# Kernel optimization log

Hardware: AMD Instinct MI355X
Metric: run time of the kernel (lower is better)

Reference implementation:

```python
import jax, jax.numpy as jnp
import numpy as np

N = 50000      # nodes
E = 1600000    # edges
D = 128        # input_dim
H = 128        # hidden_dim
C = 10         # n_class
G = 512        # number of graphs (max(idx)+1)
LRELU_ALPHA = 0.05
BN_EPS = 1e-5


def setup_inputs() -> dict:
    key = jax.random.key(0)
    ks = jax.random.split(key, 10)
    x_in = jax.random.normal(ks[0], (N, D), dtype=jnp.float32)
    edge_index = jax.random.randint(ks[1], (2, E), 0, N, dtype=jnp.int32)
    idx = jnp.sort(jax.random.randint(ks[2], (N,), 0, G, dtype=jnp.int32))

    def lin(k, shape, fan_in):
        return jax.random.normal(k, shape, dtype=jnp.float32) / np.sqrt(fan_in).astype(np.float32)

    fc_w = lin(ks[3], (H, D), D)        # GATLayer.fc weight
    a1 = lin(ks[4], (H,), 2 * H)        # a weight, src half
    a2 = lin(ks[5], (H,), 2 * H)        # a weight, dst half
    fc1_w = lin(ks[6], (H, H), H)
    fc1_b = jnp.zeros((H,), jnp.float32)
    fc2_w = lin(ks[7], (C, H), H)
    fc2_b = jnp.zeros((C,), jnp.float32)
    gamma = jnp.ones((H,), jnp.float32)  # BatchNorm weight
    beta = jnp.zeros((H,), jnp.float32)  # BatchNorm bias
    return {"x_in": x_in, "edge_index": edge_index, "idx": idx,
            "fc_w": fc_w, "a1": a1, "a2": a2,
            "fc1_w": fc1_w, "fc1_b": fc1_b, "fc2_w": fc2_w, "fc2_b": fc2_b,
            "gamma": gamma, "beta": beta}


def reference(x_in, edge_index, idx, fc_w, a1, a2, fc1_w, fc1_b, fc2_w, fc2_b, gamma, beta):
    # input standardization (torch.std is unbiased -> ddof=1)
    x = (x_in - jnp.mean(x_in)) / jnp.std(x_in, ddof=1)

    # ---- GAT layer ----
    z = x @ fc_w.T                              # [N, H]
    src, dst = edge_index[0], edge_index[1]
    # a([z_src ; z_dst]) == z_src@a1 + z_dst@a2  (avoids materializing [E, 2H])
    s1 = z @ a1                                  # [N]
    s2 = z @ a2                                  # [N]
    e = s1[src] + s2[dst]                        # [E]
    e = jnp.where(e >= 0, e, LRELU_ALPHA * e)    # LeakyReLU(0.05)
    h = jnp.exp(e)
    h_sum = jax.ops.segment_sum(h, src, num_segments=N)   # edge-softmax denom per src row
    alpha = h / h_sum[src]                       # [E]
    # sparse.mm(adj_att, z): out[src] += alpha * z[dst]
    out = jax.ops.segment_sum(alpha[:, None] * z[dst], src, num_segments=N)  # [N, H]

    x = jax.nn.relu(out)
    # dropout: identity (eval / deterministic reference)

    # sum pooling per graph
    pooled = jax.ops.segment_sum(x, idx, num_segments=G)   # [G, H]

    # BatchNorm1d (training-mode batch statistics, biased var)
    mu = jnp.mean(pooled, axis=0)
    var = jnp.var(pooled, axis=0)
    xb = (pooled - mu) / jnp.sqrt(var + BN_EPS) * gamma + beta

    x = jax.nn.relu(xb @ fc1_w.T + fc1_b)
    logits = x @ fc2_w.T + fc2_b
    return jax.nn.log_softmax(logits, axis=1)
```

## Files before the change

### kernel.cpp

```cpp
#include <hip/hip_runtime.h>

#define NN 50000
#define NE 1600000
#define DD 128
#define HH 128
#define CC 10
#define GG 512
#define LRELU_A 0.05f
#define BN_EPS 1e-5f

#define TT 256
#define EPT (NE / TT)
#define NB 196
#define NPB 256
#define KNODE 8
#define STB 1024

typedef unsigned int u32;
typedef unsigned short u16;
typedef unsigned char u8;
typedef __attribute__((ext_vector_type(8))) short bf16x8;
typedef __attribute__((ext_vector_type(4))) float f32x4;

__device__ __forceinline__ u16 f2bf(float f) {
    u32 u = __float_as_uint(f);
    u32 r = u + 0x7FFFu + ((u >> 16) & 1u);
    return (u16)(r >> 16);
}
__device__ __forceinline__ float bf2f(u32 lo16) {
    return __uint_as_float(lo16 << 16);
}

__global__ __launch_bounds__(256) void k_front(const int* __restrict__ src,
                                               const float* __restrict__ x,
                                               u16* __restrict__ cnt_b,
                                               u8* __restrict__ rank_e,
                                               float* __restrict__ pooled,
                                               double* __restrict__ pst) {
    __shared__ u32 h[NB];
    __shared__ double ls[4], lss[4];
    int bid = blockIdx.x, tid = threadIdx.x;
    if (bid < TT) {
        for (int i = tid; i < NB; i += 256) h[i] = 0;
        pooled[bid * 256 + tid] = 0.f;
        __syncthreads();
        int e0 = bid * EPT;
        for (int i = tid; i < EPT; i += 256) {
            int b = src[e0 + i] >> 8;
            u32 old = atomicAdd(&h[b], 1u);
            rank_e[e0 + i] = (u8)old;
        }
        __syncthreads();
        for (int i = tid; i < NB; i += 256) cnt_b[bid * NB + i] = (u16)h[i];
    } else {
        int sb = bid - TT;
        const int M4 = NN * DD / 4;
        double s = 0.0, ss = 0.0;
        for (int i = sb * 256 + tid; i < M4; i += STB * 256) {
            float4 v = reinterpret_cast<const float4*>(x)[i];
            s  += (double)v.x + (double)v.y + (double)v.z + (double)v.w;
            ss += (double)v.x * v.x + (double)v.y * v.y + (double)v.z * v.z +
                  (double)v.w * v.w;
        }
        for (int d = 32; d; d >>= 1) { s += __shfl_down(s, d); ss += __shfl_down(ss, d); }
        int lane = tid & 63, w = tid >> 6;
        if (lane == 0) { ls[w] = s; lss[w] = ss; }
        __syncthreads();
        if (tid == 0) {
            pst[2 * sb]     = ls[0] + ls[1] + ls[2] + ls[3];
            pst[2 * sb + 1] = lss[0] + lss[1] + lss[2] + lss[3];
        }
    }
}

__global__ __launch_bounds__(256) void k_mid(const u16* __restrict__ cnt_b,
                                             const double* __restrict__ pst,
                                             const float* __restrict__ fc_w,
                                             u16* __restrict__ rel_b,
                                             int* __restrict__ base_b,
                                             float* __restrict__ wsum,
                                             float* __restrict__ musig,
                                             u16* __restrict__ wbf) {
    int t = threadIdx.x;
    if (blockIdx.x == 0) {
        __shared__ int sm[256];
        int b = t;
        int run = 0;
        if (b < NB) {
            for (int tt = 0; tt < TT; ++tt) {
                int c = cnt_b[tt * NB + b];
                rel_b[tt * NB + b] = (u16)run;
                run += c;
            }
        }
        sm[b] = (b < NB) ? run : 0;
        __syncthreads();
        int v = sm[b];
        for (int d = 1; d < 256; d <<= 1) {
            int x = 0;
            if (b >= d) x = sm[b - d];
            __syncthreads();
            if (b >= d) sm[b] += x;
            __syncthreads();
        }
        if (b < NB) base_b[b] = sm[b] - v;
        if (b == NB - 1) base_b[NB] = sm[b];
    } else {
        __shared__ double rs[256], rss[256];
        double s  = pst[2 * t] + pst[2 * (t + 256)] + pst[2 * (t + 512)] + pst[2 * (t + 768)];
        double ss = pst[2 * t + 1] + pst[2 * (t + 256) + 1] +
                    pst[2 * (t + 512) + 1] + pst[2 * (t + 768) + 1];
        rs[t] = s; rss[t] = ss;
        __syncthreads();
        for (int d = 128; d; d >>= 1) {
            if (t < d) { rs[t] += rs[t + d]; rss[t] += rss[t + d]; }
            __syncthreads();
        }
        if (t == 0) {
            double M = (double)NN * DD;
            double mean = rs[0] / M;
            double var  = (rss[0] - rs[0] * rs[0] / M) / (M - 1.0);
            musig[0] = (float)mean;
            musig[1] = (float)(1.0 / sqrt(var));
        }
        for (int i = t; i < DD * HH; i += 256) wbf[i] = f2bf(fc_w[i]);
        if (t < 128) {
            float acc = 0.f;
            for (int k = 0; k < DD; ++k)
                acc += bf2f(f2bf(fc_w[t * DD + k]));
            wsum[t] = acc;
        }
    }
}

#define XP 136
__global__ __launch_bounds__(256) void k_big(const int* __restrict__ src,
                                             const int* __restrict__ dst,
                                             const u16* __restrict__ rel_b,
                                             const u8* __restrict__ rank_e,
                                             const int* __restrict__ base_b,
                                             u32* __restrict__ ebuf,
                                             const float* __restrict__ x,
                                             const u16* __restrict__ wbf,
                                             const float* __restrict__ wsum,
                                             const float* __restrict__ musig,
                                             const float* __restrict__ a1,
                                             const float* __restrict__ a2,
                                             u32* __restrict__ zbf,
                                             float* __restrict__ s1,
                                             float* __restrict__ s2) {
    __shared__ u16 xls[64 * XP];
    int bid = blockIdx.x, tid = threadIdx.x;

    if (bid < TT) {
        int e0 = bid * EPT;
        for (int i = tid; i < EPT; i += 256) {
            int s = src[e0 + i];
            int b = s >> 8;
            int pos = base_b[b] + (int)rel_b[bid * NB + b] + (int)rank_e[e0 + i];
            ebuf[pos] = ((u32)dst[e0 + i] << 8) | (u32)(s & 255);
        }
        return;
    }

    int row0 = (bid - TT) * 64;
    for (int i = tid; i < 64 * 32; i += 256) {
        int r = i >> 5, m = i & 31;
        int gr = row0 + r;
        float4 v = (gr < NN) ? reinterpret_cast<const float4*>(x)[gr * 32 + m]
                             : make_float4(0.f, 0.f, 0.f, 0.f);
        u32 p0 = ((u32)f2bf(v.y) << 16) | f2bf(v.x);
        u32 p1 = ((u32)f2bf(v.w) << 16) | f2bf(v.z);
        *reinterpret_cast<uint2*>(&xls[r * XP + m * 4]) = make_uint2(p0, p1);
    }
    __syncthreads();

    int w = tid >> 6, l = tid & 63;
    int lrow = l & 15, lk = l >> 4;

    bf16x8 af[4];
    #pragma unroll
    for (int kc = 0; kc < 4; ++kc)
        af[kc] = *reinterpret_cast<const bf16x8*>(
            &xls[(w * 16 + lrow) * XP + kc * 32 + lk * 8]);

    f32x4 acc[8];
    #pragma unroll
    for (int nt = 0; nt < 8; ++nt) acc[nt] = (f32x4){0.f, 0.f, 0.f, 0.f};

    #pragma unroll
    for (int nt = 0; nt < 8; ++nt) {
        #pragma unroll
        for (int kc = 0; kc < 4; ++kc) {
            bf16x8 bfr = *reinterpret_cast<const bf16x8*>(
                &wbf[(nt * 16 + lrow) * DD + kc * 32 + lk * 8]);
            acc[nt] = __builtin_amdgcn_mfma_f32_16x16x32_bf16(af[kc], bfr,
                                                              acc[nt], 0, 0, 0);
        }
    }
    __syncthreads();

    float mu = musig[0], isig = musig[1];
    #pragma unroll
    for (int nt = 0; nt < 8; ++nt) {
        int col = nt * 16 + lrow;
        float wsc = wsum[col];
        #pragma unroll
        for (int r = 0; r < 4; ++r) {
            int lr = w * 16 + lk * 4 + r;
            float z = (acc[nt][r] - mu * wsc) * isig;
            xls[lr * XP + col] = f2bf(z);
        }
    }
    __syncthreads();

    {
        int r = tid >> 2, q = tid & 3;
        int gr = row0 + r;
        const uint4* lz = reinterpret_cast<const uint4*>(&xls[r * XP + q * 32]);
        uint4 c0 = lz[0], c1 = lz[1], c2 = lz[2], c3 = lz[3];
        if (gr < NN) {
            uint4* zb = reinterpret_cast<uint4*>(zbf) + gr * 16 + q * 4;
            zb[0] = c0; zb[1] = c1; zb[2] = c2; zb[3] = c3;
        }
        u32 wd[16] = {c0.x, c0.y, c0.z, c0.w, c1.x, c1.y, c1.z, c1.w,
                      c2.x, c2.y, c2.z, c2.w, c3.x, c3.y, c3.z, c3.w};
        const float4* A14 = reinterpret_cast<const float4*>(a1 + q * 32);
        const float4* A24 = reinterpret_cast<const float4*>(a2 + q * 32);
        float p1 = 0.f, p2 = 0.f;
        #pragma unroll
        for (int j = 0; j < 8; ++j) {
            float4 va1 = A14[j], va2 = A24[j];
            u32 wlo = wd[2 * j], whi = wd[2 * j + 1];
            float z0 = bf2f(wlo & 0xFFFFu), z1 = bf2f(wlo >> 16);
            float z2 = bf2f(whi & 0xFFFFu), z3 = bf2f(whi >> 16);
            p1 += z0 * va1.x + z1 * va1.y + z2 * va1.z + z3 * va1.w;
            p2 += z0 * va2.x + z1 * va2.y + z2 * va2.z + z3 * va2.w;
        }
        p1 += __shfl_down(p1, 2, 4); p1 += __shfl_down(p1, 1, 4);
        p2 += __shfl_down(p2, 2, 4); p2 += __shfl_down(p2, 1, 4);
        if (q == 0 && gr < NN) { s1[gr] = p1; s2[gr] = p2; }
    }
}

__global__ __launch_bounds__(256) void k_bcsr(const u32* __restrict__ ebuf,
                                              const int* __restrict__ base_b,
                                              const float* __restrict__ s1,
                                              const float* __restrict__ s2,
                                              int* __restrict__ off,
                                              u32* __restrict__ dst_s) {
    __shared__ u32 hist[NPB];
    __shared__ u32 cur[NPB];
    __shared__ int sm[256];
    int b = blockIdx.x, tid = threadIdx.x;
    int ebase = base_b[b], eend = base_b[b + 1];
    int m = eend - ebase;
    hist[tid] = 0;
    __syncthreads();
    for (int i = tid; i < m; i += 256)
        atomicAdd(&hist[ebuf[ebase + i] & 255u], 1u);
    __syncthreads();
    int v = (int)hist[tid];
    sm[tid] = v;
    __syncthreads();
    for (int d = 1; d < 256; d <<= 1) {
        int x = 0;
        if (tid >= d) x = sm[tid - d];
        __syncthreads();
        if (tid >= d) sm[tid] += x;
        __syncthreads();
    }
    int st = sm[tid] - v;
    cur[tid] = (u32)st;
    int n = b * NPB + tid;
    if (n < NN) off[n] = ebase + st;
    if (b == NB - 1 && tid == 0) off[NN] = NE;
    __syncthreads();
    for (int i = tid; i < m; i += 256) {
        u32 e = ebuf[ebase + i];
        int ls = (int)(e & 255u);
        int dn = (int)(e >> 8);
        int p = (int)atomicAdd(&cur[ls], 1u);
        float ev = s1[b * NPB + ls] + s2[dn];
        ev = (ev >= 0.f) ? ev : LRELU_A * ev;
        float h = __expf(ev);
        dst_s[ebase + p] = ((u32)dn << 16) | (u32)f2bf(h);
    }
}

__global__ __launch_bounds__(256) void k_aggregate(const u32* __restrict__ zbf,
                                                   const int* __restrict__ off,
                                                   const u32* __restrict__ dst_s,
                                                   const int* __restrict__ idx,
                                                   float* __restrict__ pooled) {
    int wave = (blockIdx.x * 256 + threadIdx.x) >> 6;
    int lane = threadIdx.x & 63;
    int n0 = wave * KNODE;
    if (n0 >= NN) return;
    int n1 = n0 + KNODE;
    if (n1 > NN) n1 = NN;

    float pool0 = 0.f, pool1 = 0.f;
    int curg = idx[n0];

    for (int node = n0; node < n1; ++node) {
        int g = idx[node];
        if (g != curg) {
            atomicAdd(&pooled[curg * HH + lane * 2], pool0);
            atomicAdd(&pooled[curg * HH + lane * 2 + 1], pool1);
            pool0 = 0.f; pool1 = 0.f;
            curg = g;
        }
        int j0 = off[node], j1 = off[node + 1];
        float acc0 = 0.f, acc1 = 0.f, hsl = 0.f;

        for (int b = j0; b < j1; b += 64) {
            int cnt = j1 - b;
            if (cnt > 64) cnt = 64;
            int jj = b + ((lane < cnt) ? lane : 0);
            int ul = (int)dst_s[jj];
            if (lane < cnt) hsl += __uint_as_float((u32)ul << 16);
            int k = 0;
            for (; k + 8 <= cnt; k += 8) {
                int eu[8]; u32 uu[8];
                #pragma unroll
                for (int q = 0; q < 8; ++q) eu[q] = __shfl(ul, k + q);
                #pragma unroll
                for (int q = 0; q < 8; ++q)
                    uu[q] = zbf[(((u32)eu[q] >> 16) << 6) | lane];
                #pragma unroll
                for (int q = 0; q < 8; ++q) {
                    float hq = __uint_as_float((u32)eu[q] << 16);
                    acc0 += hq * __uint_as_float(uu[q] << 16);
                    acc1 += hq * __uint_as_float(uu[q] & 0xFFFF0000u);
                }
            }
            for (; k + 4 <= cnt; k += 4) {
                int eu[4]; u32 uu[4];
                #pragma unroll
                for (int q = 0; q < 4; ++q) eu[q] = __shfl(ul, k + q);
                #pragma unroll
                for (int q = 0; q < 4; ++q)
                    uu[q] = zbf[(((u32)eu[q] >> 16) << 6) | lane];
                #pragma unroll
                for (int q = 0; q < 4; ++q) {
                    float hq = __uint_as_float((u32)eu[q] << 16);
                    acc0 += hq * __uint_as_float(uu[q] << 16);
                    acc1 += hq * __uint_as_float(uu[q] & 0xFFFF0000u);
                }
            }
            for (; k < cnt; ++k) {
                int e = __shfl(ul, k);
                float hk = __uint_as_float((u32)e << 16);
                u32 u = zbf[(((u32)e >> 16) << 6) | lane];
                acc0 += hk * __uint_as_float(u << 16);
                acc1 += hk * __uint_as_float(u & 0xFFFF0000u);
            }
        }
        float hs = hsl;
        #pragma unroll
        for (int d = 32; d; d >>= 1) hs += __shfl_xor(hs, d);
        float inv = (hs > 0.f) ? 1.f / hs : 0.f;
        pool0 += fmaxf(acc0 * inv, 0.f);
        pool1 += fmaxf(acc1 * inv, 0.f);
    }
    atomicAdd(&pooled[curg * HH + lane * 2], pool0);
    atomicAdd(&pooled[curg * HH + lane * 2 + 1], pool1);
}

__global__ __launch_bounds__(128) void k_head(const float* __restrict__ pooled,
                                              const float* __restrict__ gamma,
                                              const float* __restrict__ beta,
                                              const float* __restrict__ fc1w,
                                              const float* __restrict__ fc1b,
                                              const float* __restrict__ fc2w,
                                              const float* __restrict__ fc2b,
                                              float* __restrict__ out) {
    __shared__ __align__(16) float xb[128];
    __shared__ __align__(16) float h1[128];
    __shared__ float lg[16];
    int g = blockIdx.x;
    int t = threadIdx.x;
    float s = 0.f, ss = 0.f;
    #pragma unroll 8
    for (int q = 0; q < GG; ++q) {
        float v = pooled[q * HH + t];
        s += v;
        ss += v * v;
    }
    float mean = s / GG;
    float var  = ss / GG - mean * mean;
    float sc = gamma[t] * rsqrtf(var + BN_EPS);
    xb[t] = pooled[g * HH + t] * sc + (beta[t] - mean * sc);
    __syncthreads();
    float acc = 0.f;
    const float4* wr = reinterpret_cast<const float4*>(&fc1w[t * HH]);
    #pragma unroll 8
    for (int k = 0; k < 32; ++k) {
        float4 w4 = wr[k];
        float4 xv = *reinterpret_cast<const float4*>(&xb[k * 4]);
        acc += w4.x * xv.x + w4.y * xv.y + w4.z * xv.z + w4.w * xv.w;
    }
    acc += fc1b[t];
    h1[t] = (acc > 0.f) ? acc : 0.f;
    __syncthreads();
    if (t < CC) {
        float a = 0.f;
        const float4* w2 = reinterpret_cast<const float4*>(&fc2w[t * HH]);
        #pragma unroll 8
        for (int k = 0; k < 32; ++k) {
            float4 w4 = w2[k];
            float4 hv = *reinterpret_cast<const float4*>(&h1[k * 4]);
            a += w4.x * hv.x + w4.y * hv.y + w4.z * hv.z + w4.w * hv.w;
        }
        lg[t] = a + fc2b[t];
    }
    __syncthreads();
    if (t == 0) {
        float mx = lg[0];
        for (int c = 1; c < CC; ++c) mx = fmaxf(mx, lg[c]);
        float se = 0.f;
        for (int c = 0; c < CC; ++c) se += __expf(lg[c] - mx);
        float lse = mx + logf(se);
        for (int c = 0; c < CC; ++c) out[g * CC + c] = lg[c] - lse;
    }
}

extern "C" void kernel_launch(void* const* d_in, const int* in_sizes, int n_in,
                              void* d_out, int out_size, void* d_ws, size_t ws_size,
                              hipStream_t stream) {
    const float* x_in  = (const float*)d_in[0];
    const int*   eidx  = (const int*)d_in[1];
    const int*   src   = eidx;
    const int*   dst   = eidx + NE;
    const int*   idx   = (const int*)d_in[2];
    const float* fc_w  = (const float*)d_in[3];
    const float* a1    = (const float*)d_in[4];
    const float* a2    = (const float*)d_in[5];
    const float* fc1w  = (const float*)d_in[6];
    const float* fc1b  = (const float*)d_in[7];
    const float* fc2w  = (const float*)d_in[8];
    const float* fc2b  = (const float*)d_in[9];
    const float* gamma = (const float*)d_in[10];
    const float* beta  = (const float*)d_in[11];
    float* out = (float*)d_out;

    char* p = (char*)d_ws;
    auto alloc = [&](size_t bytes) {
        char* r = p;
        p += (bytes + 255) & ~(size_t)255;
        return r;
    };
    double* pst    = (double*)alloc((size_t)STB * 2 * sizeof(double));
    float*  wsum   = (float*)alloc(HH * sizeof(float));
    float*  musig  = (float*)alloc(4 * sizeof(float));
    u16*    wbf    = (u16*)alloc((size_t)DD * HH * sizeof(u16));
    u16*    cnt_b  = (u16*)alloc((size_t)TT * NB * sizeof(u16));
    u16*    rel_b  = (u16*)alloc((size_t)TT * NB * sizeof(u16));
    u8*     rank_e = (u8*)alloc((size_t)NE * sizeof(u8));
    int*    base_b = (int*)alloc((NB + 1) * sizeof(int));
    u32*    ebuf   = (u32*)alloc((size_t)NE * sizeof(u32));
    int*    off    = (int*)alloc((NN + 1) * sizeof(int));
    u32*    dst_s  = (u32*)alloc((size_t)NE * sizeof(u32));
    u32*    zbf    = (u32*)alloc((size_t)NN * (HH / 2) * sizeof(u32));
    float*  s1     = (float*)alloc(NN * sizeof(float));
    float*  s2     = (float*)alloc(NN * sizeof(float));
    float*  pooled = (float*)alloc((size_t)GG * HH * sizeof(float));

    k_front<<<TT + STB, 256, 0, stream>>>(src, x_in, cnt_b, rank_e, pooled, pst);
    k_mid<<<2, 256, 0, stream>>>(cnt_b, pst, fc_w, rel_b, base_b, wsum, musig, wbf);
    int gemm_blocks = (NN + 63) / 64;
    k_big<<<TT + gemm_blocks, 256, 0, stream>>>(src, dst, rel_b, rank_e, base_b,
                                                ebuf, x_in, wbf, wsum, musig,
                                                a1, a2, zbf, s1, s2);
    k_bcsr<<<NB, 256, 0, stream>>>(ebuf, base_b, s1, s2, off, dst_s);
    int nwaves = (NN + KNODE - 1) / KNODE;
    int nblocks = (nwaves + 3) / 4;
    k_aggregate<<<nblocks, 256, 0, stream>>>(zbf, off, dst_s, idx, pooled);
    k_head<<<GG, 128, 0, stream>>>(pooled, gamma, beta, fc1w, fc1b, fc2w, fc2b, out);
}
```

Measured before the change: 171.4 us.

## Replace global per-edge rank buffer with LDS-local bucket sort before edge scatter

k_front no longer writes a per-edge rank byte array; it only builds per-block bucket histograms. The scatter blocks in k_big rebuild the histogram in shared memory, prefix-scan it, and bucket-sort the block's edges into LDS. They then write them to the global edge buffer in bucket order, so stores land in contiguous runs. This removes the global write and read of the rank array and turns scattered global writes into mostly grouped ones. The cost is a second read of src, extra shared atomics and scan barriers, and a larger static shared allocation that also applies to the GEMM blocks and may lower their occupancy.

Result: no change. 174.0 us (+1.5%).

```diff
diff --git a/kernel.cpp b/kernel.cpp
--- a/kernel.cpp
+++ b/kernel.cpp
@@ -34,7 +34,6 @@
 __global__ __launch_bounds__(256) void k_front(const int* __restrict__ src,
                                                const float* __restrict__ x,
                                                u16* __restrict__ cnt_b,
-                                               u8* __restrict__ rank_e,
                                                float* __restrict__ pooled,
                                                double* __restrict__ pst) {
     __shared__ u32 h[NB];
@@ -45,11 +44,8 @@
         pooled[bid * 256 + tid] = 0.f;
         __syncthreads();
         int e0 = bid * EPT;
-        for (int i = tid; i < EPT; i += 256) {
-            int b = src[e0 + i] >> 8;
-            u32 old = atomicAdd(&h[b], 1u);
-            rank_e[e0 + i] = (u8)old;
-        }
+        for (int i = tid; i < EPT; i += 256)
+            atomicAdd(&h[src[e0 + i] >> 8], 1u);
         __syncthreads();
         for (int i = tid; i < NB; i += 256) cnt_b[bid * NB + i] = (u16)h[i];
     } else {
@@ -134,10 +130,10 @@
 }
 
 #define XP 136
+#define SHWORDS (EPT + NB + NB + 256)
 __global__ __launch_bounds__(256) void k_big(const int* __restrict__ src,
                                              const int* __restrict__ dst,
                                              const u16* __restrict__ rel_b,
-                                             const u8* __restrict__ rank_e,
                                              const int* __restrict__ base_b,
                                              u32* __restrict__ ebuf,
                                              const float* __restrict__ x,
@@ -149,20 +145,50 @@
                                              u32* __restrict__ zbf,
                                              float* __restrict__ s1,
                                              float* __restrict__ s2) {
-    __shared__ u16 xls[64 * XP];
+    __shared__ __align__(16) u32 shmem[SHWORDS];
     int bid = blockIdx.x, tid = threadIdx.x;
 
     if (bid < TT) {
+        u32* eloc = shmem;
+        u32* hcur = shmem + EPT;
+        int* tpl  = (int*)(shmem + EPT + NB);
+        int* sm2  = (int*)(shmem + EPT + NB + NB);
         int e0 = bid * EPT;
+        for (int i = tid; i < NB; i += 256) hcur[i] = 0;
+        __syncthreads();
+        for (int i = tid; i < EPT; i += 256)
+            atomicAdd(&hcur[src[e0 + i] >> 8], 1u);
+        __syncthreads();
+        int b = tid;
+        int v = (b < NB) ? (int)hcur[b] : 0;
+        sm2[tid] = v;
+        __syncthreads();
+        for (int d = 1; d < 256; d <<= 1) {
+            int xv = 0;
+            if (tid >= d) xv = sm2[tid - d];
+            __syncthreads();
+            if (tid >= d) sm2[tid] += xv;
+            __syncthreads();
+        }
+        if (b < NB) { tpl[b] = sm2[tid] - v; hcur[b] = (u32)(sm2[tid] - v); }
+        __syncthreads();
         for (int i = tid; i < EPT; i += 256) {
             int s = src[e0 + i];
-            int b = s >> 8;
-            int pos = base_b[b] + (int)rel_b[bid * NB + b] + (int)rank_e[e0 + i];
-            ebuf[pos] = ((u32)dst[e0 + i] << 8) | (u32)(s & 255);
+            u32 pos = atomicAdd(&hcur[s >> 8], 1u);
+            eloc[pos] = ((u32)dst[e0 + i] << 16) | (u32)s;
+        }
+        __syncthreads();
+        for (int i = tid; i < EPT; i += 256) {
+            u32 e = eloc[i];
+            int s = (int)(e & 0xFFFFu);
+            int b2 = s >> 8;
+            int gpos = base_b[b2] + (int)rel_b[bid * NB + b2] + (i - tpl[b2]);
+            ebuf[gpos] = ((e >> 16) << 8) | (u32)(s & 255);
         }
         return;
     }
 
+    u16* xls = (u16*)shmem;
     int row0 = (bid - TT) * 64;
     for (int i = tid; i < 64 * 32; i += 256) {
         int r = i >> 5, m = i & 31;
@@ -457,7 +483,6 @@
     u16*    wbf    = (u16*)alloc((size_t)DD * HH * sizeof(u16));
     u16*    cnt_b  = (u16*)alloc((size_t)TT * NB * sizeof(u16));
     u16*    rel_b  = (u16*)alloc((size_t)TT * NB * sizeof(u16));
-    u8*     rank_e = (u8*)alloc((size_t)NE * sizeof(u8));
     int*    base_b = (int*)alloc((NB + 1) * sizeof(int));
     u32*    ebuf   = (u32*)alloc((size_t)NE * sizeof(u32));
     int*    off    = (int*)alloc((NN + 1) * sizeof(int));
@@ -467,10 +492,10 @@
     float*  s2     = (float*)alloc(NN * sizeof(float));
     float*  pooled = (float*)alloc((size_t)GG * HH * sizeof(float));
 
-    k_front<<<TT + STB, 256, 0, stream>>>(src, x_in, cnt_b, rank_e, pooled, pst);
+    k_front<<<TT + STB, 256, 0, stream>>>(src, x_in, cnt_b, pooled, pst);
     k_mid<<<2, 256, 0, stream>>>(cnt_b, pst, fc_w, rel_b, base_b, wsum, musig, wbf);
     int gemm_blocks = (NN + 63) / 64;
-    k_big<<<TT + gemm_blocks, 256, 0, stream>>>(src, dst, rel_b, rank_e, base_b,
+    k_big<<<TT + gemm_blocks, 256, 0, stream>>>(src, dst, rel_b, base_b,
                                                 ebuf, x_in, wbf, wsum, musig,
                                                 a1, a2, zbf, s1, s2);
     k_bcsr<<<NB, 256, 0, stream>>>(ebuf, base_b, s1, s2, off, dst_s);
```

## Fuse block CSR build and neighbor aggregation into one LDS-resident kernel

Applied to the files above, without the earlier changes.

Replaces the separate CSR-building kernel and aggregation kernel with one 1024-thread kernel per 256-node block. Each block buckets its edges and computes the attention weights into shared memory, then aggregates straight from that local sorted edge list. This removes the global write and re-read of the sorted edge array, the offset array and one launch. In exchange the aggregation runs on only 196 large blocks, which is fewer than the number of compute units and means fewer waves to hide gather latency. It also assumes each block has at most 8832 edges, with no bounds check.

Result: no change. 171.5 us (+0.0%).

```diff
diff --git a/kernel.cpp b/kernel.cpp
--- a/kernel.cpp
+++ b/kernel.cpp
@@ -13,7 +13,7 @@
 #define EPT (NE / TT)
 #define NB 196
 #define NPB 256
-#define KNODE 8
+#define EMAXB 8832
 #define STB 1024
 
 typedef unsigned int u32;
@@ -243,67 +243,67 @@
     }
 }
 
-__global__ __launch_bounds__(256) void k_bcsr(const u32* __restrict__ ebuf,
-                                              const int* __restrict__ base_b,
-                                              const float* __restrict__ s1,
-                                              const float* __restrict__ s2,
-                                              int* __restrict__ off,
-                                              u32* __restrict__ dst_s) {
+__global__ __launch_bounds__(1024) void k_agg2(const u32* __restrict__ ebuf,
+                                               const int* __restrict__ base_b,
+                                               const float* __restrict__ s1,
+                                               const float* __restrict__ s2,
+                                               const u32* __restrict__ zbf,
+                                               const int* __restrict__ idx,
+                                               float* __restrict__ pooled) {
+    __shared__ u32 eloc[EMAXB];
     __shared__ u32 hist[NPB];
     __shared__ u32 cur[NPB];
-    __shared__ int sm[256];
+    __shared__ int sm[NPB];
+    __shared__ int off_l[NPB + 1];
     int b = blockIdx.x, tid = threadIdx.x;
-    int ebase = base_b[b], eend = base_b[b + 1];
-    int m = eend - ebase;
-    hist[tid] = 0;
-    __syncthreads();
-    for (int i = tid; i < m; i += 256)
+    int ebase = base_b[b];
+    int m = base_b[b + 1] - ebase;
+
+    if (tid < NPB) hist[tid] = 0;
+    __syncthreads();
+    for (int i = tid; i < m; i += 1024)
         atomicAdd(&hist[ebuf[ebase + i] & 255u], 1u);
     __syncthreads();
-    int v = (int)hist[tid];
-    sm[tid] = v;
-    __syncthreads();
-    for (int d = 1; d < 256; d <<= 1) {
+    if (tid < NPB) sm[tid] = (int)hist[tid];
+    __syncthreads();
+    for (int d = 1; d < NPB; d <<= 1) {
         int x = 0;
-        if (tid >= d) x = sm[tid - d];
-        __syncthreads();
-        if (tid >= d) sm[tid] += x;
-        __syncthreads();
-    }
-    int st = sm[tid] - v;
-    cur[tid] = (u32)st;
-    int n = b * NPB + tid;
-    if (n < NN) off[n] = ebase + st;
-    if (b == NB - 1 && tid == 0) off[NN] = NE;
-    __syncthreads();
-    for (int i = tid; i < m; i += 256) {
+        if (tid < NPB && tid >= d) x = sm[tid - d];
+        __syncthreads();
+        if (tid < NPB && tid >= d) sm[tid] += x;
+        __syncthreads();
+    }
+    if (tid < NPB) {
+        int v = (int)hist[tid];
+        int st = sm[tid] - v;
+        cur[tid] = (u32)st;
+        off_l[tid] = st;
+    }
+    if (tid == 0) off_l[NPB] = m;
+    __syncthreads();
+    for (int i = tid; i < m; i += 1024) {
         u32 e = ebuf[ebase + i];
         int ls = (int)(e & 255u);
         int dn = (int)(e >> 8);
         int p = (int)atomicAdd(&cur[ls], 1u);
         float ev = s1[b * NPB + ls] + s2[dn];
         ev = (ev >= 0.f) ? ev : LRELU_A * ev;
-        float h = __expf(ev);
-        dst_s[ebase + p] = ((u32)dn << 16) | (u32)f2bf(h);
-    }
-}
-
-__global__ __launch_bounds__(256) void k_aggregate(const u32* __restrict__ zbf,
-                                                   const int* __restrict__ off,
-                                                   const u32* __restrict__ dst_s,
-                                                   const int* __restrict__ idx,
-                                                   float* __restrict__ pooled) {
-    int wave = (blockIdx.x * 256 + threadIdx.x) >> 6;
-    int lane = threadIdx.x & 63;
-    int n0 = wave * KNODE;
-    if (n0 >= NN) return;
-    int n1 = n0 + KNODE;
-    if (n1 > NN) n1 = NN;
+        eloc[p] = ((u32)dn << 16) | (u32)f2bf(__expf(ev));
+    }
+    __syncthreads();
+
+    int w = tid >> 6, lane = tid & 63;
+    int ln0 = w * 16;
+    int gn0 = b * NPB + ln0;
+    if (gn0 >= NN) return;
 
     float pool0 = 0.f, pool1 = 0.f;
-    int curg = idx[n0];
-
-    for (int node = n0; node < n1; ++node) {
+    int curg = idx[gn0];
+
+    for (int q16 = 0; q16 < 16; ++q16) {
+        int ln = ln0 + q16;
+        int node = b * NPB + ln;
+        if (node >= NN) break;
         int g = idx[node];
         if (g != curg) {
             atomicAdd(&pooled[curg * HH + lane * 2], pool0);
@@ -311,14 +311,14 @@
             pool0 = 0.f; pool1 = 0.f;
             curg = g;
         }
-        int j0 = off[node], j1 = off[node + 1];
+        int j0 = off_l[ln], j1 = off_l[ln + 1];
         float acc0 = 0.f, acc1 = 0.f, hsl = 0.f;
 
-        for (int b = j0; b < j1; b += 64) {
-            int cnt = j1 - b;
+        for (int bb = j0; bb < j1; bb += 64) {
+            int cnt = j1 - bb;
             if (cnt > 64) cnt = 64;
-            int jj = b + ((lane < cnt) ? lane : 0);
-            int ul = (int)dst_s[jj];
+            int jj = bb + ((lane < cnt) ? lane : 0);
+            int ul = (int)eloc[jj];
             if (lane < cnt) hsl += __uint_as_float((u32)ul << 16);
             int k = 0;
             for (; k + 8 <= cnt; k += 8) {
@@ -460,8 +460,6 @@
     u8*     rank_e = (u8*)alloc((size_t)NE * sizeof(u8));
     int*    base_b = (int*)alloc((NB + 1) * sizeof(int));
     u32*    ebuf   = (u32*)alloc((size_t)NE * sizeof(u32));
-    int*    off    = (int*)alloc((NN + 1) * sizeof(int));
-    u32*    dst_s  = (u32*)alloc((size_t)NE * sizeof(u32));
     u32*    zbf    = (u32*)alloc((size_t)NN * (HH / 2) * sizeof(u32));
     float*  s1     = (float*)alloc(NN * sizeof(float));
     float*  s2     = (float*)alloc(NN * sizeof(float));
@@ -473,9 +471,6 @@
     k_big<<<TT + gemm_blocks, 256, 0, stream>>>(src, dst, rel_b, rank_e, base_b,
                                                 ebuf, x_in, wbf, wsum, musig,
                                                 a1, a2, zbf, s1, s2);
-    k_bcsr<<<NB, 256, 0, stream>>>(ebuf, base_b, s1, s2, off, dst_s);
-    int nwaves = (NN + KNODE - 1) / KNODE;
-    int nblocks = (nwaves + 3) / 4;
-    k_aggregate<<<nblocks, 256, 0, stream>>>(zbf, off, dst_s, idx, pooled);
+    k_agg2<<<NB, 1024, 0, stream>>>(ebuf, base_b, s1, s2, zbf, idx, pooled);
     k_head<<<GG, 128, 0, stream>>>(pooled, gamma, beta, fc1w, fc1b, fc2w, fc2b, out);
 }
```
